# Optimization experiments

Hardware: AMD Instinct MI355X
Metric: run time of the kernel (lower is better)

The kernel has to match this reference:

```python
import jax, jax.numpy as jnp
import numpy as np

B, S, D = 2, 2048, 1024
H = 16
HD = D // H  # 64
SCALE = 1.0 / np.sqrt(HD)


def setup_inputs() -> dict:
    key = jax.random.key(0)
    k1, k2, k3, k4, k5 = jax.random.split(key, 5)
    std = 0.02
    return {
        "Q_input": jax.random.normal(k1, (B, S, D), dtype=jnp.float32),
        "Wq": jax.random.normal(k2, (D, H * HD), dtype=jnp.float32) * std,
        "Wk": jax.random.normal(k3, (D, HD), dtype=jnp.float32) * std,
        "Wv": jax.random.normal(k4, (D, HD), dtype=jnp.float32) * std,
        "Wo": jax.random.normal(k5, (H * HD, D), dtype=jnp.float32) * std,
    }


def reference(Q_input, Wq, Wk, Wv, Wo):
    b, s, _ = Q_input.shape
    # projections; K/V use a single shared head (MQA)
    Q = (Q_input @ Wq).reshape(b, s, H, HD)   # [b,s,H,hd]
    K = Q_input @ Wk                           # [b,s,hd]
    V = Q_input @ Wv                           # [b,s,hd]
    # scores: broadcast the single KV head across all H query heads
    scores = jnp.einsum("bqhd,bkd->bhqk", Q, K) * SCALE  # [b,H,s,s]
    probs = jax.nn.softmax(scores, axis=-1)
    ctx = jnp.einsum("bhqk,bkd->bqhd", probs, V)          # [b,s,H,hd]
    out = ctx.reshape(b, s, H * HD) @ Wo                  # [b,s,D]
    return out
```

## Files before the change

### kernel.cpp

```cpp
#include <hip/hip_runtime.h>

typedef __attribute__((ext_vector_type(8))) short bf16x8;
typedef __attribute__((ext_vector_type(4))) float f32x4;
typedef __attribute__((ext_vector_type(4))) unsigned int u32x4;
typedef unsigned short u16;

#define MFMA16(a,b,c) __builtin_amdgcn_mfma_f32_16x16x32_bf16((a),(b),(c),0,0,0)

__device__ __forceinline__ u16 f2bf(float f){
  unsigned int u = __float_as_uint(f);
  u += 0x7fffu + ((u >> 16) & 1u);
  return (u16)(u >> 16);
}
__device__ __forceinline__ float bf2f(u16 v){
  return __uint_as_float(((unsigned int)v) << 16);
}
__device__ __forceinline__ unsigned int cvtpk(float lo, float hi){
  unsigned int r;
  asm("v_cvt_pk_bf16_f32 %0, %1, %2" : "=v"(r) : "v"(lo), "v"(hi));
  return r;
}
__device__ __forceinline__ void gload16(const void* g, void* l){
  __builtin_amdgcn_global_load_lds(
      (__attribute__((address_space(1))) void*)g,
      (__attribute__((address_space(3))) void*)l, 16, 0, 0);
}

__global__ __launch_bounds__(256) void mqa_tcvt4(
    const float* __restrict__ Wq, const float* __restrict__ Wk,
    const float* __restrict__ Wv, const float* __restrict__ Wo,
    u16* __restrict__ WT, u16* __restrict__ WoT)
{
  __shared__ float t[32][33];
  int bx = blockIdx.x;
  const float* src; u16* dst; int C, cb, rb;
  if (bx < 1024)      { src = Wq; dst = WT;                      C = 1024; int q = bx;        cb = q & 31; rb = q >> 5; }
  else if (bx < 1088) { src = Wk; dst = WT + (size_t)1024*1024;  C = 64;   int q = bx - 1024; cb = q & 1;  rb = q >> 1; }
  else if (bx < 1152) { src = Wv; dst = WT + (size_t)1088*1024;  C = 64;   int q = bx - 1088; cb = q & 1;  rb = q >> 1; }
  else                { src = Wo; dst = WoT;                     C = 1024; int q = bx - 1152; cb = q & 31; rb = q >> 5; }
  int c0 = cb * 32, r0 = rb * 32;
  int x = threadIdx.x & 31, y0 = threadIdx.x >> 5;
  #pragma unroll
  for (int yy = y0; yy < 32; yy += 8)
    t[yy][x] = src[(size_t)(r0 + yy) * C + c0 + x];
  __syncthreads();
  #pragma unroll
  for (int yy = y0; yy < 32; yy += 8)
    dst[(size_t)(c0 + yy) * 1024 + r0 + x] = f2bf(t[x][yy]);
}

template<int MODE>
__global__ __launch_bounds__(256, 3) void mqa_gemm(
    const float* __restrict__ Af, const u16* __restrict__ Op,
    const float* __restrict__ Lp, const u16* __restrict__ Bt,
    float* __restrict__ outF, u16* __restrict__ Qb, u16* __restrict__ Kb,
    u16* __restrict__ Vtb, int M, int N, int K, int NT)
{
  __shared__ __align__(16) u16 lds_a[2][64*64];
  __shared__ __align__(16) u16 lds_b[2][128*64];
  int nwg = gridDim.x;
  int bx = ((int)blockIdx.x & 7) * (nwg >> 3) + ((int)blockIdx.x >> 3);
  int mt = bx / NT, nt = bx % NT;
  int m0 = mt * 64, n0 = nt * 128;
  int tid = threadIdx.x;
  int wid = tid >> 6, lane = tid & 63;
  int wr = (wid >> 1) * 32, wc = (wid & 1) * 64;
  int fr = lane & 15, g = lane >> 4;
  int sw = fr & 7;

  int ar = tid >> 2, ac = (tid & 3) * 16;
  int m_a = m0 + ar;
  int ab = m_a >> 11, as_ = m_a & 2047;
  int c8a = ac >> 3, rw8 = ar & 7;
  int srow = lane >> 3;
  int scol = ((lane & 7) ^ srow) * 8;

  f32x4 acc[2][4];
  #pragma unroll
  for (int i = 0; i < 2; ++i)
    #pragma unroll
    for (int j = 0; j < 4; ++j) acc[i][j] = (f32x4)0.f;

  float4 fA[4];
  bf16x8 pA0, pA1, pB0, pB1;
  float rlA = 0.f;

  auto loadA = [&](int k0){
    if (MODE == 1) {
      const float* src = &Af[(size_t)m_a * K + k0 + ac];
      fA[0] = *(const float4*)(src);
      fA[1] = *(const float4*)(src + 4);
      fA[2] = *(const float4*)(src + 8);
      fA[3] = *(const float4*)(src + 12);
    } else {
      int h = k0 >> 6;
      float l0 = Lp[(((size_t)(ab*2    ))*16 + h)*2048 + as_];
      float l1 = Lp[(((size_t)(ab*2 + 1))*16 + h)*2048 + as_];
      rlA = 1.f / (l0 + l1);
      const u16* p0 = &Op[(((size_t)(ab*2    ))*2048 + as_)*1024 + k0 + ac];
      const u16* p1 = &Op[(((size_t)(ab*2 + 1))*2048 + as_)*1024 + k0 + ac];
      pA0 = *(const bf16x8*)p0; pA1 = *(const bf16x8*)(p0 + 8);
      pB0 = *(const bf16x8*)p1; pB1 = *(const bf16x8*)(p1 + 8);
    }
  };

  auto writeA = [&](int bi){
    unsigned int w0[4], w1[4];
    if (MODE == 1) {
      w0[0] = cvtpk(fA[0].x, fA[0].y); w0[1] = cvtpk(fA[0].z, fA[0].w);
      w0[2] = cvtpk(fA[1].x, fA[1].y); w0[3] = cvtpk(fA[1].z, fA[1].w);
      w1[0] = cvtpk(fA[2].x, fA[2].y); w1[1] = cvtpk(fA[2].z, fA[2].w);
      w1[2] = cvtpk(fA[3].x, fA[3].y); w1[3] = cvtpk(fA[3].z, fA[3].w);
    } else {
      #pragma unroll
      for (int j = 0; j < 4; ++j) {
        float e0 = (bf2f((u16)pA0[2*j  ]) + bf2f((u16)pB0[2*j  ])) * rlA;
        float e1 = (bf2f((u16)pA0[2*j+1]) + bf2f((u16)pB0[2*j+1])) * rlA;
        w0[j] = cvtpk(e0, e1);
        float e2 = (bf2f((u16)pA1[2*j  ]) + bf2f((u16)pB1[2*j  ])) * rlA;
        float e3 = (bf2f((u16)pA1[2*j+1]) + bf2f((u16)pB1[2*j+1])) * rlA;
        w1[j] = cvtpk(e2, e3);
      }
    }
    u32x4 v0 = { w0[0], w0[1], w0[2], w0[3] };
    u32x4 v1 = { w1[0], w1[1], w1[2], w1[3] };
    *(bf16x8*)&lds_a[bi][ar*64 + ((c8a    ) ^ rw8)*8] = __builtin_bit_cast(bf16x8, v0);
    *(bf16x8*)&lds_a[bi][ar*64 + ((c8a + 1) ^ rw8)*8] = __builtin_bit_cast(bf16x8, v1);
  };

  auto stageB = [&](int bi, int k0){
    #pragma unroll
    for (int cc = 0; cc < 4; ++cc) {
      int rb = (wid*4 + cc) * 8;
      gload16(&Bt[(size_t)(n0 + rb + srow) * K + k0 + scol], &lds_b[bi][rb*64]);
    }
  };

  loadA(0);
  stageB(0, 0);
  writeA(0);
  __syncthreads();

  int cur = 0;
  for (int k0 = 0; k0 < K; k0 += 64) {
    bool nx = (k0 + 64 < K);
    if (nx) { loadA(k0 + 64); stageB(cur ^ 1, k0 + 64); }
    #pragma unroll
    for (int ks = 0; ks < 2; ++ks) {
      bf16x8 af[2], bfr[4];
      #pragma unroll
      for (int i = 0; i < 2; ++i)
        af[i] = *(const bf16x8*)&lds_a[cur][(wr + i*16 + fr)*64 + (((ks*4+g) ^ sw))*8];
      #pragma unroll
      for (int j = 0; j < 4; ++j)
        bfr[j] = *(const bf16x8*)&lds_b[cur][(wc + j*16 + fr)*64 + (((ks*4+g) ^ sw))*8];
      #pragma unroll
      for (int i = 0; i < 2; ++i)
        #pragma unroll
        for (int j = 0; j < 4; ++j)
          acc[i][j] = MFMA16(af[i], bfr[j], acc[i][j]);
    }
    if (nx) writeA(cur ^ 1);
    __syncthreads();
    cur ^= 1;
  }

  int fg = g;
  #pragma unroll
  for (int i = 0; i < 2; ++i) {
    #pragma unroll
    for (int j = 0; j < 4; ++j) {
      int ncol = n0 + wc + j*16 + fr;
      #pragma unroll
      for (int r = 0; r < 4; ++r) {
        int m = m0 + wr + i*16 + fg*4 + r;
        float v = acc[i][j][r];
        if (MODE == 2) {
          outF[(size_t)m * N + ncol] = v;
        } else {
          u16 bv = f2bf(v);
          if (ncol < 1024) {
            Qb[(size_t)m * 1024 + ncol] = bv;
          } else if (ncol < 1088) {
            Kb[(size_t)m * 64 + (ncol - 1024)] = bv;
          } else {
            int b = m >> 11, s = m & 2047;
            int k = s & 63;
            int pos = (k & 35) | ((k & 12) << 1) | ((k & 16) >> 2);
            Vtb[((size_t)b * 64 + (ncol - 1088)) * 2048 + (s & ~63) + pos] = bv;
          }
        }
      }
    }
  }
}

__global__ __launch_bounds__(256, 4) void mqa_attn(
    const u16* __restrict__ Qb, const u16* __restrict__ Kb,
    const u16* __restrict__ Vtb, u16* __restrict__ Opart,
    float* __restrict__ Lpart)
{
  const float C1 = 0.18033688011112042f;
  const float MC = 32.f * C1;
  int qt = blockIdx.x, h = blockIdx.y;
  int b = blockIdx.z >> 1, sp = blockIdx.z & 1;
  int part = blockIdx.z;
  int tid = threadIdx.x, wid = tid >> 6, lane = tid & 63;
  int fr = lane & 15, g = lane >> 4;
  int q0 = qt * 128 + wid * 32;

  __shared__ __align__(16) u16 KT[2][64*64];
  __shared__ __align__(16) u16 VT[2][64*64];

  const u16* Qbase = Qb + (size_t)b * 2048 * 1024 + (size_t)h * 64;
  const u16* Kbase = Kb + (size_t)b * 2048 * 64;
  const u16* Vbase = Vtb + (size_t)b * 64 * 2048;

  int srow = lane >> 3;
  int scol = ((lane & 7) ^ srow) * 8;

  bf16x8 qfv[2][2];
  #pragma unroll
  for (int qf_ = 0; qf_ < 2; ++qf_)
    #pragma unroll
    for (int ks = 0; ks < 2; ++ks)
      qfv[qf_][ks] = *(const bf16x8*)&Qbase[(size_t)(q0 + qf_*16 + fr) * 1024 + ks*32 + g*8];

  f32x4 oacc[2][4];
  #pragma unroll
  for (int qf_ = 0; qf_ < 2; ++qf_)
    #pragma unroll
    for (int vf = 0; vf < 4; ++vf) oacc[qf_][vf] = (f32x4)0.f;
  float lacc0 = 0.f, lacc1 = 0.f;

  const int kb0 = sp * 16;

  #pragma unroll
  for (int j = 0; j < 2; ++j) {
    int row = wid*16 + j*8 + srow;
    gload16(&Kbase[(size_t)(kb0*64 + row) * 64 + scol], &KT[0][(wid*16 + j*8) * 64]);
    gload16(&Vbase[(size_t)row * 2048 + kb0*64 + scol], &VT[0][(wid*16 + j*8) * 64]);
  }
  __syncthreads();

  int cur = 0;
  for (int kb = kb0; kb < kb0 + 16; ++kb) {
    if (kb + 1 < kb0 + 16) {
      int ntl = kb + 1;
      #pragma unroll
      for (int j = 0; j < 2; ++j) {
        int row = wid*16 + j*8 + srow;
        gload16(&Kbase[(size_t)(ntl*64 + row) * 64 + scol], &KT[cur^1][(wid*16 + j*8) * 64]);
        gload16(&Vbase[(size_t)row * 2048 + ntl*64 + scol], &VT[cur^1][(wid*16 + j*8) * 64]);
      }
    }

    const u16* kc = &KT[cur][0];
    const u16* vc = &VT[cur][0];

    f32x4 sacc[2][4];
    #pragma unroll
    for (int qf_ = 0; qf_ < 2; ++qf_)
      #pragma unroll
      for (int kf = 0; kf < 4; ++kf) sacc[qf_][kf] = (f32x4)0.f;

    __builtin_amdgcn_s_setprio(1);
    #pragma unroll
    for (int ks = 0; ks < 2; ++ks) {
      #pragma unroll
      for (int kf = 0; kf < 4; ++kf) {
        bf16x8 kfr = *(const bf16x8*)&kc[(kf*16 + fr)*64 + (((ks*4+g) ^ (fr&7)))*8];
        sacc[0][kf] = MFMA16(kfr, qfv[0][ks], sacc[0][kf]);
        sacc[1][kf] = MFMA16(kfr, qfv[1][ks], sacc[1][kf]);
      }
    }
    __builtin_amdgcn_s_setprio(0);

    unsigned int pk0[8], pk1[8];
    float s0 = 0.f, s1 = 0.f;
    #pragma unroll
    for (int kf = 0; kf < 4; ++kf) {
      float a0 = __builtin_amdgcn_exp2f(sacc[0][kf][0] * C1 - MC);
      float a1 = __builtin_amdgcn_exp2f(sacc[0][kf][1] * C1 - MC);
      float a2 = __builtin_amdgcn_exp2f(sacc[0][kf][2] * C1 - MC);
      float a3 = __builtin_amdgcn_exp2f(sacc[0][kf][3] * C1 - MC);
      s0 += (a0 + a1) + (a2 + a3);
      pk0[2*kf]   = cvtpk(a0, a1);
      pk0[2*kf+1] = cvtpk(a2, a3);
      float b0 = __builtin_amdgcn_exp2f(sacc[1][kf][0] * C1 - MC);
      float b1 = __builtin_amdgcn_exp2f(sacc[1][kf][1] * C1 - MC);
      float b2 = __builtin_amdgcn_exp2f(sacc[1][kf][2] * C1 - MC);
      float b3 = __builtin_amdgcn_exp2f(sacc[1][kf][3] * C1 - MC);
      s1 += (b0 + b1) + (b2 + b3);
      pk1[2*kf]   = cvtpk(b0, b1);
      pk1[2*kf+1] = cvtpk(b2, b3);
    }
    lacc0 += s0;
    lacc1 += s1;

    __builtin_amdgcn_s_setprio(1);
    #pragma unroll
    for (int ks2 = 0; ks2 < 2; ++ks2) {
      u32x4 w0 = { pk0[4*ks2], pk0[4*ks2+1], pk0[4*ks2+2], pk0[4*ks2+3] };
      u32x4 w1 = { pk1[4*ks2], pk1[4*ks2+1], pk1[4*ks2+2], pk1[4*ks2+3] };
      bf16x8 pA0 = __builtin_bit_cast(bf16x8, w0);
      bf16x8 pA1 = __builtin_bit_cast(bf16x8, w1);
      #pragma unroll
      for (int vf = 0; vf < 4; ++vf) {
        bf16x8 vfr = *(const bf16x8*)&vc[(vf*16 + fr)*64 + (((ks2*4+g) ^ (fr&7)))*8];
        oacc[0][vf] = MFMA16(pA0, vfr, oacc[0][vf]);
        oacc[1][vf] = MFMA16(pA1, vfr, oacc[1][vf]);
      }
    }
    __builtin_amdgcn_s_setprio(0);

    __syncthreads();
    cur ^= 1;
  }

  lacc0 += __shfl_xor(lacc0, 16); lacc0 += __shfl_xor(lacc0, 32);
  lacc1 += __shfl_xor(lacc1, 16); lacc1 += __shfl_xor(lacc1, 32);

  #pragma unroll
  for (int qf_ = 0; qf_ < 2; ++qf_) {
    #pragma unroll
    for (int r = 0; r < 4; ++r) {
      int row = q0 + qf_*16 + g*4 + r;
      #pragma unroll
      for (int vf = 0; vf < 4; ++vf) {
        int col = h*64 + vf*16 + fr;
        Opart[((size_t)part * 2048 + row) * 1024 + col] = f2bf(oacc[qf_][vf][r]);
      }
    }
  }
  if (g == 0) {
    int q = q0 + fr;
    size_t base = ((size_t)part * 16 + h) * 2048;
    Lpart[base + q]      = lacc0;
    Lpart[base + q + 16] = lacc1;
  }
}

extern "C" void kernel_launch(void* const* d_in, const int* in_sizes, int n_in,
                              void* d_out, int out_size, void* d_ws, size_t ws_size,
                              hipStream_t stream)
{
  const float* Qin = (const float*)d_in[0];
  const float* Wq  = (const float*)d_in[1];
  const float* Wk  = (const float*)d_in[2];
  const float* Wv  = (const float*)d_in[3];
  const float* Wo  = (const float*)d_in[4];
  float* out = (float*)d_out;

  u16* WoT = (u16*)d_ws;
  u16* Qb  = WoT + (size_t)1024*1024;
  u16* Kb  = Qb  + (size_t)4096*1024;
  u16* Vtb = Kb  + (size_t)4096*64;
  float* Lpart = (float*)(Vtb + (size_t)2*64*2048);
  u16* WT    = (u16*)(Lpart + (size_t)4*16*2048);
  u16* Opart = WT;

  mqa_tcvt4<<<2176, 256, 0, stream>>>(Wq, Wk, Wv, Wo, WT, WoT);

  mqa_gemm<1><<<64*9, 256, 0, stream>>>(Qin, nullptr, nullptr, WT,
                                        nullptr, Qb, Kb, Vtb,
                                        4096, 1152, 1024, 9);
  mqa_attn<<<dim3(16,16,4), 256, 0, stream>>>(Qb, Kb, Vtb, Opart, Lpart);
  mqa_gemm<2><<<64*8, 256, 0, stream>>>(nullptr, Opart, Lpart, WoT,
                                        out, nullptr, nullptr, nullptr,
                                        4096, 1024, 1024, 8);
}
```

Measured before the change: 102.6 us.

## Load fp32 A operand directly into MFMA fragments, bypassing LDS in projection GEMM

In the QKV projection GEMM (MODE 1), each wave now loads its own fp32 A rows straight from global memory in MFMA fragment layout and converts them to bf16 in registers, instead of staging the converted tile through LDS. This removes the LDS writes and reads for A and shrinks its LDS allocation, which may allow more resident workgroups. In exchange, the two waves that share an A row block each load those rows from global memory, so A global traffic doubles. Each lane also fetches 32-byte row segments, which is a less coalesced pattern and holds more registers.

```diff
diff --git a/kernel.cpp b/kernel.cpp
--- a/kernel.cpp
+++ b/kernel.cpp
@@ -56,7 +56,7 @@
     float* __restrict__ outF, u16* __restrict__ Qb, u16* __restrict__ Kb,
     u16* __restrict__ Vtb, int M, int N, int K, int NT)
 {
-  __shared__ __align__(16) u16 lds_a[2][64*64];
+  __shared__ __align__(16) u16 lds_a[2][(MODE == 2) ? 64*64 : 8];
   __shared__ __align__(16) u16 lds_b[2][128*64];
   int nwg = gridDim.x;
   int bx = ((int)blockIdx.x & 7) * (nwg >> 3) + ((int)blockIdx.x >> 3);
@@ -81,17 +81,20 @@
     #pragma unroll
     for (int j = 0; j < 4; ++j) acc[i][j] = (f32x4)0.f;
 
-  float4 fA[4];
+  float4 rA[4][2];
   bf16x8 pA0, pA1, pB0, pB1;
   float rlA = 0.f;
 
   auto loadA = [&](int k0){
     if (MODE == 1) {
-      const float* src = &Af[(size_t)m_a * K + k0 + ac];
-      fA[0] = *(const float4*)(src);
-      fA[1] = *(const float4*)(src + 4);
-      fA[2] = *(const float4*)(src + 8);
-      fA[3] = *(const float4*)(src + 12);
+      #pragma unroll
+      for (int i = 0; i < 2; ++i)
+        #pragma unroll
+        for (int ks = 0; ks < 2; ++ks) {
+          const float* rp = &Af[(size_t)(m0 + wr + i*16 + fr) * K + k0 + ks*32 + g*8];
+          rA[i*2+ks][0] = *(const float4*)rp;
+          rA[i*2+ks][1] = *(const float4*)(rp + 4);
+        }
     } else {
       int h = k0 >> 6;
       float l0 = Lp[(((size_t)(ab*2    ))*16 + h)*2048 + as_];
@@ -106,21 +109,14 @@
 
   auto writeA = [&](int bi){
     unsigned int w0[4], w1[4];
-    if (MODE == 1) {
-      w0[0] = cvtpk(fA[0].x, fA[0].y); w0[1] = cvtpk(fA[0].z, fA[0].w);
-      w0[2] = cvtpk(fA[1].x, fA[1].y); w0[3] = cvtpk(fA[1].z, fA[1].w);
-      w1[0] = cvtpk(fA[2].x, fA[2].y); w1[1] = cvtpk(fA[2].z, fA[2].w);
-      w1[2] = cvtpk(fA[3].x, fA[3].y); w1[3] = cvtpk(fA[3].z, fA[3].w);
-    } else {
-      #pragma unroll
-      for (int j = 0; j < 4; ++j) {
-        float e0 = (bf2f((u16)pA0[2*j  ]) + bf2f((u16)pB0[2*j  ])) * rlA;
-        float e1 = (bf2f((u16)pA0[2*j+1]) + bf2f((u16)pB0[2*j+1])) * rlA;
-        w0[j] = cvtpk(e0, e1);
-        float e2 = (bf2f((u16)pA1[2*j  ]) + bf2f((u16)pB1[2*j  ])) * rlA;
-        float e3 = (bf2f((u16)pA1[2*j+1]) + bf2f((u16)pB1[2*j+1])) * rlA;
-        w1[j] = cvtpk(e2, e3);
-      }
+    #pragma unroll
+    for (int j = 0; j < 4; ++j) {
+      float e0 = (bf2f((u16)pA0[2*j  ]) + bf2f((u16)pB0[2*j  ])) * rlA;
+      float e1 = (bf2f((u16)pA0[2*j+1]) + bf2f((u16)pB0[2*j+1])) * rlA;
+      w0[j] = cvtpk(e0, e1);
+      float e2 = (bf2f((u16)pA1[2*j  ]) + bf2f((u16)pB1[2*j  ])) * rlA;
+      float e3 = (bf2f((u16)pA1[2*j+1]) + bf2f((u16)pB1[2*j+1])) * rlA;
+      w1[j] = cvtpk(e2, e3);
     }
     u32x4 v0 = { w0[0], w0[1], w0[2], w0[3] };
     u32x4 v1 = { w1[0], w1[1], w1[2], w1[3] };
@@ -138,29 +134,40 @@
 
   loadA(0);
   stageB(0, 0);
-  writeA(0);
+  if (MODE == 2) writeA(0);
   __syncthreads();
 
   int cur = 0;
   for (int k0 = 0; k0 < K; k0 += 64) {
     bool nx = (k0 + 64 < K);
+    bf16x8 af[4];
+    if (MODE == 1) {
+      #pragma unroll
+      for (int f = 0; f < 4; ++f) {
+        u32x4 v = { cvtpk(rA[f][0].x, rA[f][0].y), cvtpk(rA[f][0].z, rA[f][0].w),
+                    cvtpk(rA[f][1].x, rA[f][1].y), cvtpk(rA[f][1].z, rA[f][1].w) };
+        af[f] = __builtin_bit_cast(bf16x8, v);
+      }
+    }
     if (nx) { loadA(k0 + 64); stageB(cur ^ 1, k0 + 64); }
     #pragma unroll
     for (int ks = 0; ks < 2; ++ks) {
-      bf16x8 af[2], bfr[4];
-      #pragma unroll
-      for (int i = 0; i < 2; ++i)
-        af[i] = *(const bf16x8*)&lds_a[cur][(wr + i*16 + fr)*64 + (((ks*4+g) ^ sw))*8];
+      bf16x8 a0, a1, bfr[4];
+      if (MODE == 1) { a0 = af[ks]; a1 = af[2+ks]; }
+      else {
+        a0 = *(const bf16x8*)&lds_a[cur][(wr      + fr)*64 + (((ks*4+g) ^ sw))*8];
+        a1 = *(const bf16x8*)&lds_a[cur][(wr + 16 + fr)*64 + (((ks*4+g) ^ sw))*8];
+      }
       #pragma unroll
       for (int j = 0; j < 4; ++j)
         bfr[j] = *(const bf16x8*)&lds_b[cur][(wc + j*16 + fr)*64 + (((ks*4+g) ^ sw))*8];
       #pragma unroll
-      for (int i = 0; i < 2; ++i)
-        #pragma unroll
-        for (int j = 0; j < 4; ++j)
-          acc[i][j] = MFMA16(af[i], bfr[j], acc[i][j]);
-    }
-    if (nx) writeA(cur ^ 1);
+      for (int j = 0; j < 4; ++j) {
+        acc[0][j] = MFMA16(a0, bfr[j], acc[0][j]);
+        acc[1][j] = MFMA16(a1, bfr[j], acc[1][j]);
+      }
+    }
+    if (MODE == 2 && nx) writeA(cur ^ 1);
     __syncthreads();
     cur ^= 1;
   }
```

New measurement: 132.2 us. +28.8%, slower.
